# Kernel tuning notes

Hardware: AMD Instinct MI355X
Metric: run time of the kernel (lower is better)

Reference implementation:

```python
import jax, jax.numpy as jnp
import numpy as np

B, S, E = 4096, 128, 768   # batch, seq_len, bert hidden
HID = 384                  # mlp_dims[-1]
NH = 9                     # num_head (domains)
NE = 5                     # num_expert (hardcoded in module)


def setup_inputs() -> dict:
    key = jax.random.key(0)
    ks = jax.random.split(key, 14)
    std = 0.02
    return {
        "feature": jax.random.normal(ks[0], (B, S, E), dtype=jnp.float32),
        "masks": jax.random.randint(ks[1], (B, S), 0, 2, dtype=jnp.int32),
        "category": jax.random.randint(ks[2], (B,), 0, NH, dtype=jnp.int32),
        # MaskAttention: Linear(E, 1)
        "attn_w": jax.random.normal(ks[3], (E,), dtype=jnp.float32) * std,
        "attn_b": jnp.zeros((), dtype=jnp.float32),
        # gates: per-head Sequential(Linear(E,HID), ReLU, Linear(HID,NE), Softmax)
        "gate_w1": jax.random.normal(ks[4], (NH, E, HID), dtype=jnp.float32) * std,
        "gate_b1": jnp.zeros((NH, HID), dtype=jnp.float32),
        "gate_w2": jax.random.normal(ks[5], (NH, HID, NE), dtype=jnp.float32) * std,
        "gate_b2": jnp.zeros((NH, NE), dtype=jnp.float32),
        # experts: MLP(E, [HID]) = Linear(E,HID) + ReLU (dropout inactive in eval)
        "expert_w": jax.random.normal(ks[6], (NE, E, HID), dtype=jnp.float32) * std,
        "expert_b": jnp.zeros((NE, HID), dtype=jnp.float32),
        # heads: per-head Linear(HID, 1)
        "head_w": jax.random.normal(ks[7], (NH, HID), dtype=jnp.float32) * std,
        "head_b": jnp.zeros((NH,), dtype=jnp.float32),
    }


def reference(feature, masks, category, attn_w, attn_b,
              gate_w1, gate_b1, gate_w2, gate_b2,
              expert_w, expert_b, head_w, head_b):
    # ---- MaskAttention pooling: scores = Linear(E,1)(feature), mask, softmax over S
    scores = jnp.einsum('bse,e->bs', feature, attn_w) + attn_b          # [B,S]
    scores = jnp.where(masks == 0, jnp.float32(-1e9), scores)
    alpha = jax.nn.softmax(scores, axis=-1)                             # [B,S]
    pooled = jnp.einsum('bs,bse->be', alpha, feature)                   # [B,E]

    b_idx = jnp.arange(pooled.shape[0])

    # ---- category-indexed gate: compute all NH gate MLPs, select per sample
    gh = jax.nn.relu(jnp.einsum('be,heo->hbo', pooled, gate_w1) + gate_b1[:, None, :])
    glog = jnp.einsum('hbo,hok->hbk', gh, gate_w2) + gate_b2[:, None, :]
    gates_all = jax.nn.softmax(glog, axis=-1)                           # [NH,B,NE]
    gate_value = gates_all[category, b_idx]                             # [B,NE]

    # ---- experts: rep = sum_k gate[:,k] * relu(pooled @ Wk + bk)
    eh = jax.nn.relu(jnp.einsum('be,keo->kbo', pooled, expert_w) + expert_b[:, None, :])
    rep = jnp.einsum('bk,kbo->bo', gate_value, eh)                      # [B,HID]

    # ---- category-indexed head: per-sample Linear(HID,1)
    out = jnp.sum(rep * head_w[category], axis=-1) + head_b[category]   # [B]
    return jax.nn.sigmoid(out)
```

## Files before the change

kernel.cpp:

```cpp
#include <hip/hip_runtime.h>
#include <hip/hip_bf16.h>

#define Bn   4096
#define Sn   128
#define En   768
#define HIDn 384
#define NHn  9
#define NEn  5
#define MAXTILES 41

typedef __attribute__((ext_vector_type(8))) short short8;
typedef __attribute__((ext_vector_type(4))) float f32x4;

__device__ __forceinline__ unsigned short f2bf(float v) {
  unsigned int x = __float_as_uint(v);
  x += 0x7fffu + ((x >> 16) & 1u);
  return (unsigned short)(x >> 16);
}
__device__ __forceinline__ float dot4(float4 a, float4 b) {
  return fmaf(a.x, b.x, fmaf(a.y, b.y, fmaf(a.z, b.z, a.w * b.w)));
}
__device__ __forceinline__ void fma4(float4& p, float w, float4 v) {
  p.x = fmaf(w, v.x, p.x); p.y = fmaf(w, v.y, p.y);
  p.z = fmaf(w, v.z, p.z); p.w = fmaf(w, v.w, p.w);
}

__global__ __launch_bounds__(256) void prep_kernel(
    const float* __restrict__ feature, const int* __restrict__ masks,
    const float* __restrict__ attn_w, const float* __restrict__ ew,
    const float* __restrict__ g1, const int* __restrict__ category,
    unsigned short* __restrict__ pooled, unsigned short* __restrict__ Bpe,
    unsigned short* __restrict__ Bpg, int* __restrict__ rowsamp,
    int* __restrict__ meta) {
  __shared__ __align__(16) union {
    struct { float pbuf[4][768]; float sbuf[4]; } pool;
    struct { int hist[NHn][256]; int padbase[NHn]; int total[NHn];
             int tilecat[MAXTILES]; int padTiles; } srt;
  } sm;
  const int t = threadIdx.x, lane = t & 63, wid = t >> 6;
  const int bid = blockIdx.x;

  if (bid < Bn) {
    const int b = bid;
    const float4* aw = (const float4*)attn_w;
    const float4 aw0 = aw[lane], aw1 = aw[64 + lane], aw2 = aw[128 + lane];
    const float4* fb = (const float4*)(feature + (size_t)b * (Sn * En));
    unsigned long long bal = __ballot(lane < 32 && masks[b * Sn + wid * 32 + (lane & 31)] != 0);
    unsigned int m = (unsigned int)bal;
    float4 p0 = {0,0,0,0}, p1 = {0,0,0,0}, p2 = {0,0,0,0};
    float lsum = 0.f;
    if (m) {
      int s = __builtin_ctz(m); m &= m - 1;
      const float4* rp = fb + (wid * 32 + s) * (En / 4);
      float4 c0 = rp[lane], c1 = rp[64 + lane], c2 = rp[128 + lane];
      while (m) {
        int s2 = __builtin_ctz(m); m &= m - 1;
        const float4* rp2 = fb + (wid * 32 + s2) * (En / 4);
        float4 n0 = rp2[lane], n1 = rp2[64 + lane], n2 = rp2[128 + lane];
        float part = dot4(c0, aw0) + dot4(c1, aw1) + dot4(c2, aw2);
        #pragma unroll
        for (int off = 32; off; off >>= 1) part += __shfl_xor(part, off);
        float w = __expf(part);
        lsum += w;
        fma4(p0, w, c0); fma4(p1, w, c1); fma4(p2, w, c2);
        c0 = n0; c1 = n1; c2 = n2;
      }
      float part = dot4(c0, aw0) + dot4(c1, aw1) + dot4(c2, aw2);
      #pragma unroll
      for (int off = 32; off; off >>= 1) part += __shfl_xor(part, off);
      float w = __expf(part);
      lsum += w;
      fma4(p0, w, c0); fma4(p1, w, c1); fma4(p2, w, c2);
    }
    ((float4*)sm.pool.pbuf[wid])[lane] = p0;
    ((float4*)sm.pool.pbuf[wid])[64 + lane] = p1;
    ((float4*)sm.pool.pbuf[wid])[128 + lane] = p2;
    if (lane == 0) sm.pool.sbuf[wid] = lsum;
    __syncthreads();
    float total = sm.pool.sbuf[0] + sm.pool.sbuf[1] + sm.pool.sbuf[2] + sm.pool.sbuf[3];
    if (total == 0.f) {
      p0 = p1 = p2 = float4{0,0,0,0};
      for (int s = 0; s < 32; ++s) {
        const float4* rp = fb + (wid * 32 + s) * (En / 4);
        fma4(p0, 1.f, rp[lane]); fma4(p1, 1.f, rp[64 + lane]); fma4(p2, 1.f, rp[128 + lane]);
      }
      ((float4*)sm.pool.pbuf[wid])[lane] = p0;
      ((float4*)sm.pool.pbuf[wid])[64 + lane] = p1;
      ((float4*)sm.pool.pbuf[wid])[128 + lane] = p2;
      __syncthreads();
      total = 128.f;
    }
    const float inv = 1.f / total;
    if (t < 192) {
      float4 s0 = ((const float4*)sm.pool.pbuf[0])[t];
      float4 s1 = ((const float4*)sm.pool.pbuf[1])[t];
      float4 s2 = ((const float4*)sm.pool.pbuf[2])[t];
      float4 s3 = ((const float4*)sm.pool.pbuf[3])[t];
      ushort4 u;
      u.x = f2bf((s0.x+s1.x+s2.x+s3.x) * inv);
      u.y = f2bf((s0.y+s1.y+s2.y+s3.y) * inv);
      u.z = f2bf((s0.z+s1.z+s2.z+s3.z) * inv);
      u.w = f2bf((s0.w+s1.w+s2.w+s3.w) * inv);
      ((ushort4*)pooled)[(size_t)b * 192 + t] = u;
    }
    return;
  }

  if (bid < Bn + 2016) {
    const int pair = (bid - Bn) * 4 + wid;
    const int q = lane >> 4, j = lane & 15;
    const float* src; unsigned short* dst; int kt;
    if (pair < 2880) {
      int nt = pair / 24; kt = pair % 24;
      int col = nt * 16 + j;
      src = ew + (size_t)(col / HIDn) * (En * HIDn) + (col % HIDn);
      dst = Bpe + (size_t)pair * 512;
    } else {
      int g = pair - 2880;
      int h = g / 576, rem = g % 576;
      int nt = rem / 24; kt = rem % 24;
      int col = nt * 16 + j;
      src = g1 + (size_t)h * (En * HIDn) + col;
      dst = Bpg + ((size_t)(h * 24 + nt) * 24 + kt) * 512;
    }
    unsigned short outv[8] __attribute__((aligned(16)));
    #pragma unroll
    for (int e = 0; e < 8; ++e) {
      int k = kt * 32 + q * 8 + e;
      outv[e] = f2bf(src[(size_t)k * HIDn]);
    }
    *(uint4*)&dst[lane * 8] = *(const uint4*)outv;
    return;
  }

  #pragma unroll
  for (int jj = 0; jj < NHn; ++jj) sm.srt.hist[jj][t] = 0;
  __syncthreads();
  for (int i = 0; i < 16; ++i) { int c = category[t * 16 + i]; sm.srt.hist[c][t]++; }
  __syncthreads();
  if (t < NHn) {
    int run = 0;
    for (int x = 0; x < 256; ++x) { int v = sm.srt.hist[t][x]; sm.srt.hist[t][x] = run; run += v; }
    sm.srt.total[t] = run;
  }
  __syncthreads();
  if (t == 0) {
    int pb = 0, mt = 0;
    for (int jj = 0; jj < NHn; ++jj) {
      sm.srt.padbase[jj] = pb;
      int tot = sm.srt.total[jj];
      int nt = (tot + 127) >> 7;
      for (int k2 = 0; k2 < nt; ++k2) {
        meta[1 + mt + k2] = jj;
        int vv = tot - (k2 << 7); if (vv > 128) vv = 128;
        meta[64 + mt + k2] = vv;
        sm.srt.tilecat[mt + k2] = jj;
      }
      mt += nt; pb += nt << 7;
    }
    meta[0] = mt; sm.srt.padTiles = mt;
  }
  __syncthreads();
  const int padM = sm.srt.padTiles << 7;
  for (int mm = t; mm < padM; mm += 256) {
    int h = sm.srt.tilecat[mm >> 7];
    if (mm - sm.srt.padbase[h] >= sm.srt.total[h]) rowsamp[mm] = 0;
  }
  for (int i = 0; i < 16; ++i) {
    int idx = t * 16 + i; int c = category[idx];
    int off = sm.srt.hist[c][t]++;
    rowsamp[sm.srt.padbase[c] + off] = idx;
  }
}

__global__ __launch_bounds__(256) void gemm_kernel(
    const unsigned short* __restrict__ pooled, const unsigned short* __restrict__ Bpe,
    const unsigned short* __restrict__ Bpg, const float* __restrict__ eb,
    const float* __restrict__ gb1, const float* __restrict__ g2,
    const int* __restrict__ category, const float* __restrict__ hw,
    const int* __restrict__ rowsamp, const int* __restrict__ meta,
    float* __restrict__ partial, float* __restrict__ glogp) {
  __shared__ __align__(16) struct {
    unsigned short Alds[128 * 40];
    unsigned short Blds[8 * 512];
    union {
      struct { float hwlds[NHn * HIDn]; float plds[2][128]; } e;
      struct { int rs[128]; float w2lds[640]; } g;
    } u;
  } sm;
  const int t = threadIdx.x, lane = t & 63, wid = t >> 6;
  const int wm = wid >> 1, wn = wid & 1;
  const int bid = blockIdx.x;
  const int r = t >> 2, c0 = (t & 3) * 8;
  const int arow = wm * 64 + (lane & 15);
  const int aq = (lane >> 4) * 8;
  const int lrb = wm * 64 + ((lane >> 4) << 2);
  const int cb = wn * 64 + (lane & 15);
  f32x4 acc[4][4] = {};

  if (bid < 480) {
    const int bx = bid % 15, by = bid / 15;
    const int m0 = by * 128, ntg0 = bx * 8;
    for (int idx = t; idx < NHn * HIDn; idx += 256) sm.u.e.hwlds[idx] = hw[idx];
    for (int kt = 0; kt < 24; ++kt) {
      __syncthreads();
      *(uint4*)&sm.Alds[r * 40 + c0] =
          *(const uint4*)&pooled[(size_t)(m0 + r) * En + kt * 32 + c0];
      *(uint4*)&sm.Alds[(r + 64) * 40 + c0] =
          *(const uint4*)&pooled[(size_t)(m0 + r + 64) * En + kt * 32 + c0];
      #pragma unroll
      for (int rnd = 0; rnd < 2; ++rnd) {
        int chunk = t + rnd * 256;
        int nt = chunk >> 6, l2 = chunk & 63;
        *(uint4*)&sm.Blds[nt * 512 + l2 * 8] =
            *(const uint4*)&Bpe[((size_t)(ntg0 + nt) * 24 + kt) * 512 + l2 * 8];
      }
      __syncthreads();
      short8 af[4], bfv[4];
      #pragma unroll
      for (int i = 0; i < 4; ++i) af[i] = *(const short8*)&sm.Alds[(arow + i * 16) * 40 + aq];
      #pragma unroll
      for (int i = 0; i < 4; ++i) bfv[i] = *(const short8*)&sm.Blds[(wn * 4 + i) * 512 + lane * 8];
      #pragma unroll
      for (int i = 0; i < 4; ++i)
        #pragma unroll
        for (int jj = 0; jj < 4; ++jj)
          acc[i][jj] = __builtin_amdgcn_mfma_f32_16x16x32_bf16(af[i], bfv[jj], acc[i][jj], 0, 0, 0);
    }
    const int kexp = bx / 3, lcolbase = (bx % 3) * 128;
    (void)kexp;
    float sums[4][4];
    #pragma unroll
    for (int i = 0; i < 4; ++i) {
      #pragma unroll
      for (int rr = 0; rr < 4; ++rr) {
        const int row = m0 + lrb + i * 16 + rr;
        const int cat = category[row];
        float s = 0.f;
        #pragma unroll
        for (int jj = 0; jj < 4; ++jj) {
          int cl = cb + jj * 16;
          float v = acc[i][jj][rr] + eb[bx * 128 + cl];
          v = fmaxf(v, 0.f);
          s = fmaf(v, sm.u.e.hwlds[cat * HIDn + lcolbase + cl], s);
        }
        #pragma unroll
        for (int off = 8; off; off >>= 1) s += __shfl_xor(s, off);
        sums[i][rr] = s;
      }
    }
    __syncthreads();
    if ((lane & 15) == 0) {
      #pragma unroll
      for (int i = 0; i < 4; ++i)
        #pragma unroll
        for (int rr = 0; rr < 4; ++rr)
          sm.u.e.plds[wn][lrb + i * 16 + rr] = sums[i][rr];
    }
    __syncthreads();
    if (t < 128) partial[(size_t)bx * Bn + m0 + t] = sm.u.e.plds[0][t] + sm.u.e.plds[1][t];
    return;
  }

  const int gid = bid - 480;
  const int mt = gid / 3, bxg = gid % 3;
  if (mt >= meta[0]) return;
  const int h = meta[1 + mt], valid = meta[64 + mt];
  if (t < 128) sm.u.g.rs[t] = rowsamp[mt * 128 + t];
  const float* w2src = g2 + ((size_t)h * HIDn + bxg * 128) * 5;
  for (int idx = t; idx < 640; idx += 256) sm.u.g.w2lds[idx] = w2src[idx];
  for (int kt = 0; kt < 24; ++kt) {
    __syncthreads();
    *(uint4*)&sm.Alds[r * 40 + c0] =
        *(const uint4*)&pooled[(size_t)sm.u.g.rs[r] * En + kt * 32 + c0];
    *(uint4*)&sm.Alds[(r + 64) * 40 + c0] =
        *(const uint4*)&pooled[(size_t)sm.u.g.rs[r + 64] * En + kt * 32 + c0];
    #pragma unroll
    for (int rnd = 0; rnd < 2; ++rnd) {
      int chunk = t + rnd * 256;
      int nt = chunk >> 6, l2 = chunk & 63;
      *(uint4*)&sm.Blds[nt * 512 + l2 * 8] =
          *(const uint4*)&Bpg[((size_t)(h * 24 + bxg * 8 + nt) * 24 + kt) * 512 + l2 * 8];
    }
    __syncthreads();
    short8 af[4], bfv[4];
    #pragma unroll
    for (int i = 0; i < 4; ++i) af[i] = *(const short8*)&sm.Alds[(arow + i * 16) * 40 + aq];
    #pragma unroll
    for (int i = 0; i < 4; ++i) bfv[i] = *(const short8*)&sm.Blds[(wn * 4 + i) * 512 + lane * 8];
    #pragma unroll
    for (int i = 0; i < 4; ++i)
      #pragma unroll
      for (int jj = 0; jj < 4; ++jj)
        acc[i][jj] = __builtin_amdgcn_mfma_f32_16x16x32_bf16(af[i], bfv[jj], acc[i][jj], 0, 0, 0);
  }
  #pragma unroll
  for (int i = 0; i < 4; ++i) {
    #pragma unroll
    for (int rr = 0; rr < 4; ++rr) {
      const int lrow = lrb + i * 16 + rr;
      float s[5] = {0.f, 0.f, 0.f, 0.f, 0.f};
      #pragma unroll
      for (int jj = 0; jj < 4; ++jj) {
        int cl = cb + jj * 16;
        float v = acc[i][jj][rr] + gb1[h * HIDn + bxg * 128 + cl];
        v = fmaxf(v, 0.f);
        #pragma unroll
        for (int k = 0; k < 5; ++k) s[k] = fmaf(v, sm.u.g.w2lds[cl * 5 + k], s[k]);
      }
      #pragma unroll
      for (int k = 0; k < 5; ++k)
        #pragma unroll
        for (int off = 8; off; off >>= 1) s[k] += __shfl_xor(s[k], off);
      if ((lane & 15) == 0 && lrow < valid) {
        int samp = sm.u.g.rs[lrow];
        #pragma unroll
        for (int k = 0; k < 5; ++k)
          glogp[((size_t)bxg * Bn + samp) * 5 + k] = s[k];
      }
    }
  }
}

__global__ __launch_bounds__(256) void final_kernel(
    const float* __restrict__ partial, const float* __restrict__ glogp,
    const float* __restrict__ gb2, const int* __restrict__ category,
    const float* __restrict__ hb, float* __restrict__ out) {
  const int row = blockIdx.x * 256 + threadIdx.x;
  const int cat = category[row];
  float gl[5];
  #pragma unroll
  for (int k = 0; k < 5; ++k)
    gl[k] = gb2[cat * 5 + k]
          + glogp[((size_t)0 * Bn + row) * 5 + k]
          + glogp[((size_t)1 * Bn + row) * 5 + k]
          + glogp[((size_t)2 * Bn + row) * 5 + k];
  float mx = fmaxf(fmaxf(fmaxf(gl[0], gl[1]), fmaxf(gl[2], gl[3])), gl[4]);
  float ek[5], es = 0.f;
  #pragma unroll
  for (int k = 0; k < 5; ++k) { ek[k] = __expf(gl[k] - mx); es += ek[k]; }
  const float einv = 1.f / es;
  float s = 0.f;
  #pragma unroll
  for (int k = 0; k < 5; ++k) {
    float ps = partial[(size_t)(3 * k) * Bn + row]
             + partial[(size_t)(3 * k + 1) * Bn + row]
             + partial[(size_t)(3 * k + 2) * Bn + row];
    s = fmaf(ek[k] * einv, ps, s);
  }
  s += hb[cat];
  out[row] = 1.f / (1.f + __expf(-s));
}

extern "C" void kernel_launch(void* const* d_in, const int* in_sizes, int n_in,
                              void* d_out, int out_size, void* d_ws, size_t ws_size,
                              hipStream_t stream) {
  const float* feature  = (const float*)d_in[0];
  const int*   masks    = (const int*)d_in[1];
  const int*   category = (const int*)d_in[2];
  const float* attn_w   = (const float*)d_in[3];
  const float* gate_w1  = (const float*)d_in[5];
  const float* gate_b1  = (const float*)d_in[6];
  const float* gate_w2  = (const float*)d_in[7];
  const float* gate_b2  = (const float*)d_in[8];
  const float* expert_w = (const float*)d_in[9];
  const float* expert_b = (const float*)d_in[10];
  const float* head_w   = (const float*)d_in[11];
  const float* head_b   = (const float*)d_in[12];
  float* out = (float*)d_out;

  char* ws = (char*)d_ws;
  unsigned short* pooled = (unsigned short*)(ws);
  unsigned short* Bpe    = (unsigned short*)(ws + 6291456);
  unsigned short* Bpg    = (unsigned short*)(ws + 9240576);
  int* rowsamp           = (int*)(ws + 14548992);
  int* meta              = (int*)(ws + 14569984);
  float* glogp           = (float*)(ws + 14570496);
  float* partial         = (float*)(ws + 14816256);

  prep_kernel<<<dim3(Bn + 2016 + 1), dim3(256), 0, stream>>>(
      feature, masks, attn_w, expert_w, gate_w1, category,
      pooled, Bpe, Bpg, rowsamp, meta);
  gemm_kernel<<<dim3(480 + 3 * MAXTILES), dim3(256), 0, stream>>>(
      pooled, Bpe, Bpg, expert_b, gate_b1, gate_w2, category, head_w,
      rowsamp, meta, partial, glogp);
  final_kernel<<<dim3(16), dim3(256), 0, stream>>>(
      partial, glogp, gate_b2, category, head_b, out);
}
```

Baseline: 218.4 us.

## Fuse prep and GEMM into persistent kernel with atomic work queues and flags

Replaces the separate prep and GEMM launches with one persistent kernel of 768 blocks. Blocks pull work from atomic counters: first weight packing and the category sort, then attention pooling, then GEMM tiles. Each expert GEMM tile spin-waits on a per-row-tile flag, so it can start as soon as its 128 pooled rows are ready. The goal is to overlap the tail of pooling with the GEMM and remove a launch boundary, at the cost of atomic and spin-wait overhead and lower occupancy from the larger shared-memory union.

```diff
diff --git a/kernel.cpp b/kernel.cpp
--- a/kernel.cpp
+++ b/kernel.cpp
@@ -8,6 +8,14 @@
 #define NHn  9
 #define NEn  5
 #define MAXTILES 41
+#define NBLK 768
+
+#define F_PACKDONE 0
+#define F_POOLALL  1
+#define F_TILE     2
+#define F_TPREP    34
+#define F_TPOOL    35
+#define F_TGEMM    36
 
 typedef __attribute__((ext_vector_type(8))) short short8;
 typedef __attribute__((ext_vector_type(4))) float f32x4;
@@ -24,24 +32,120 @@
   p.x = fmaf(w, v.x, p.x); p.y = fmaf(w, v.y, p.y);
   p.z = fmaf(w, v.z, p.z); p.w = fmaf(w, v.w, p.w);
 }
-
-__global__ __launch_bounds__(256) void prep_kernel(
+__device__ __forceinline__ int aload(int* p) {
+  return __hip_atomic_load(p, __ATOMIC_ACQUIRE, __HIP_MEMORY_SCOPE_AGENT);
+}
+__device__ __forceinline__ int aadd(int* p, int v) {
+  return __hip_atomic_fetch_add(p, v, __ATOMIC_RELEASE, __HIP_MEMORY_SCOPE_AGENT);
+}
+
+union SM {
+  struct { float pbuf[4][768]; float sbuf[4]; } pool;
+  struct { int hist[NHn][256]; int padbase[NHn]; int total[NHn];
+           int tilecat[MAXTILES]; int padTiles; } srt;
+  struct { unsigned short Alds[128 * 40]; unsigned short Blds[8 * 512];
+           union { struct { float hwlds[NHn * HIDn]; float plds[2][128]; } e;
+                   struct { int rs[128]; float w2lds[640]; } g; } u; } gemm;
+};
+
+__global__ void zero_kernel(int* __restrict__ flags) { flags[threadIdx.x] = 0; }
+
+__global__ __launch_bounds__(256, 2) void mega_kernel(
     const float* __restrict__ feature, const int* __restrict__ masks,
     const float* __restrict__ attn_w, const float* __restrict__ ew,
     const float* __restrict__ g1, const int* __restrict__ category,
+    const float* __restrict__ gb1, const float* __restrict__ g2,
+    const float* __restrict__ eb, const float* __restrict__ hw,
     unsigned short* __restrict__ pooled, unsigned short* __restrict__ Bpe,
     unsigned short* __restrict__ Bpg, int* __restrict__ rowsamp,
-    int* __restrict__ meta) {
-  __shared__ __align__(16) union {
-    struct { float pbuf[4][768]; float sbuf[4]; } pool;
-    struct { int hist[NHn][256]; int padbase[NHn]; int total[NHn];
-             int tilecat[MAXTILES]; int padTiles; } srt;
-  } sm;
+    int* __restrict__ meta, float* __restrict__ partial,
+    float* __restrict__ glogp, int* __restrict__ flags) {
+  __shared__ SM sm;
+  __shared__ int curu;
   const int t = threadIdx.x, lane = t & 63, wid = t >> 6;
-  const int bid = blockIdx.x;
-
-  if (bid < Bn) {
-    const int b = bid;
+
+  int nmine = 0;
+  for (;;) {
+    __syncthreads();
+    if (t == 0) curu = __hip_atomic_fetch_add(&flags[F_TPREP], 1, __ATOMIC_RELAXED, __HIP_MEMORY_SCOPE_AGENT);
+    __syncthreads();
+    const int u = curu;
+    if (u >= 2017) break;
+    ++nmine;
+    if (u < 2016) {
+      const int pair = u * 4 + wid;
+      const int q = lane >> 4, j = lane & 15;
+      const float* src; unsigned short* dst; int kt;
+      if (pair < 2880) {
+        int nt = pair / 24; kt = pair % 24;
+        int col = nt * 16 + j;
+        src = ew + (size_t)(col / HIDn) * (En * HIDn) + (col % HIDn);
+        dst = Bpe + (size_t)pair * 512;
+      } else {
+        int g = pair - 2880;
+        int h = g / 576, rem = g % 576;
+        int nt = rem / 24; kt = rem % 24;
+        int col = nt * 16 + j;
+        src = g1 + (size_t)h * (En * HIDn) + col;
+        dst = Bpg + ((size_t)(h * 24 + nt) * 24 + kt) * 512;
+      }
+      unsigned short outv[8] __attribute__((aligned(16)));
+      #pragma unroll
+      for (int e = 0; e < 8; ++e) {
+        int k = kt * 32 + q * 8 + e;
+        outv[e] = f2bf(src[(size_t)k * HIDn]);
+      }
+      *(uint4*)&dst[lane * 8] = *(const uint4*)outv;
+    } else {
+      #pragma unroll
+      for (int jj = 0; jj < NHn; ++jj) sm.srt.hist[jj][t] = 0;
+      __syncthreads();
+      for (int i = 0; i < 16; ++i) { int c = category[t * 16 + i]; sm.srt.hist[c][t]++; }
+      __syncthreads();
+      if (t < NHn) {
+        int run = 0;
+        for (int x = 0; x < 256; ++x) { int v = sm.srt.hist[t][x]; sm.srt.hist[t][x] = run; run += v; }
+        sm.srt.total[t] = run;
+      }
+      __syncthreads();
+      if (t == 0) {
+        int pb = 0, mt = 0;
+        for (int jj = 0; jj < NHn; ++jj) {
+          sm.srt.padbase[jj] = pb;
+          int tot = sm.srt.total[jj];
+          int nt = (tot + 127) >> 7;
+          for (int k2 = 0; k2 < nt; ++k2) {
+            meta[1 + mt + k2] = jj;
+            int vv = tot - (k2 << 7); if (vv > 128) vv = 128;
+            meta[64 + mt + k2] = vv;
+            sm.srt.tilecat[mt + k2] = jj;
+          }
+          mt += nt; pb += nt << 7;
+        }
+        meta[0] = mt; sm.srt.padTiles = mt;
+      }
+      __syncthreads();
+      const int padM = sm.srt.padTiles << 7;
+      for (int mm = t; mm < padM; mm += 256) {
+        int h = sm.srt.tilecat[mm >> 7];
+        if (mm - sm.srt.padbase[h] >= sm.srt.total[h]) rowsamp[mm] = 0;
+      }
+      for (int i = 0; i < 16; ++i) {
+        int idx = t * 16 + i; int c = category[idx];
+        int off = sm.srt.hist[c][t]++;
+        rowsamp[sm.srt.padbase[c] + off] = idx;
+      }
+    }
+  }
+  __syncthreads();
+  if (t == 0) { __threadfence(); aadd(&flags[F_PACKDONE], nmine); }
+
+  for (;;) {
+    __syncthreads();
+    if (t == 0) curu = __hip_atomic_fetch_add(&flags[F_TPOOL], 1, __ATOMIC_RELAXED, __HIP_MEMORY_SCOPE_AGENT);
+    __syncthreads();
+    const int b = curu;
+    if (b >= Bn) break;
     const float4* aw = (const float4*)attn_w;
     const float4 aw0 = aw[lane], aw1 = aw[64 + lane], aw2 = aw[128 + lane];
     const float4* fb = (const float4*)(feature + (size_t)b * (Sn * En));
@@ -96,227 +200,165 @@
       float4 s1 = ((const float4*)sm.pool.pbuf[1])[t];
       float4 s2 = ((const float4*)sm.pool.pbuf[2])[t];
       float4 s3 = ((const float4*)sm.pool.pbuf[3])[t];
-      ushort4 u;
-      u.x = f2bf((s0.x+s1.x+s2.x+s3.x) * inv);
-      u.y = f2bf((s0.y+s1.y+s2.y+s3.y) * inv);
-      u.z = f2bf((s0.z+s1.z+s2.z+s3.z) * inv);
-      u.w = f2bf((s0.w+s1.w+s2.w+s3.w) * inv);
-      ((ushort4*)pooled)[(size_t)b * 192 + t] = u;
-    }
-    return;
+      ushort4 u4;
+      u4.x = f2bf((s0.x+s1.x+s2.x+s3.x) * inv);
+      u4.y = f2bf((s0.y+s1.y+s2.y+s3.y) * inv);
+      u4.z = f2bf((s0.z+s1.z+s2.z+s3.z) * inv);
+      u4.w = f2bf((s0.w+s1.w+s2.w+s3.w) * inv);
+      ((ushort4*)pooled)[(size_t)b * 192 + t] = u4;
+    }
+    __syncthreads();
+    if (t == 0) {
+      __threadfence();
+      aadd(&flags[F_TILE + (b >> 7)], 1);
+      aadd(&flags[F_POOLALL], 1);
+    }
   }
 
-  if (bid < Bn + 2016) {
-    const int pair = (bid - Bn) * 4 + wid;
-    const int q = lane >> 4, j = lane & 15;
-    const float* src; unsigned short* dst; int kt;
-    if (pair < 2880) {
-      int nt = pair / 24; kt = pair % 24;
-      int col = nt * 16 + j;
-      src = ew + (size_t)(col / HIDn) * (En * HIDn) + (col % HIDn);
-      dst = Bpe + (size_t)pair * 512;
-    } else {
-      int g = pair - 2880;
-      int h = g / 576, rem = g % 576;
-      int nt = rem / 24; kt = rem % 24;
-      int col = nt * 16 + j;
-      src = g1 + (size_t)h * (En * HIDn) + col;
-      dst = Bpg + ((size_t)(h * 24 + nt) * 24 + kt) * 512;
-    }
-    unsigned short outv[8] __attribute__((aligned(16)));
-    #pragma unroll
-    for (int e = 0; e < 8; ++e) {
-      int k = kt * 32 + q * 8 + e;
-      outv[e] = f2bf(src[(size_t)k * HIDn]);
-    }
-    *(uint4*)&dst[lane * 8] = *(const uint4*)outv;
-    return;
-  }
-
-  #pragma unroll
-  for (int jj = 0; jj < NHn; ++jj) sm.srt.hist[jj][t] = 0;
-  __syncthreads();
-  for (int i = 0; i < 16; ++i) { int c = category[t * 16 + i]; sm.srt.hist[c][t]++; }
-  __syncthreads();
-  if (t < NHn) {
-    int run = 0;
-    for (int x = 0; x < 256; ++x) { int v = sm.srt.hist[t][x]; sm.srt.hist[t][x] = run; run += v; }
-    sm.srt.total[t] = run;
-  }
-  __syncthreads();
-  if (t == 0) {
-    int pb = 0, mt = 0;
-    for (int jj = 0; jj < NHn; ++jj) {
-      sm.srt.padbase[jj] = pb;
-      int tot = sm.srt.total[jj];
-      int nt = (tot + 127) >> 7;
-      for (int k2 = 0; k2 < nt; ++k2) {
-        meta[1 + mt + k2] = jj;
-        int vv = tot - (k2 << 7); if (vv > 128) vv = 128;
-        meta[64 + mt + k2] = vv;
-        sm.srt.tilecat[mt + k2] = jj;
-      }
-      mt += nt; pb += nt << 7;
-    }
-    meta[0] = mt; sm.srt.padTiles = mt;
-  }
-  __syncthreads();
-  const int padM = sm.srt.padTiles << 7;
-  for (int mm = t; mm < padM; mm += 256) {
-    int h = sm.srt.tilecat[mm >> 7];
-    if (mm - sm.srt.padbase[h] >= sm.srt.total[h]) rowsamp[mm] = 0;
-  }
-  for (int i = 0; i < 16; ++i) {
-    int idx = t * 16 + i; int c = category[idx];
-    int off = sm.srt.hist[c][t]++;
-    rowsamp[sm.srt.padbase[c] + off] = idx;
-  }
-}
-
-__global__ __launch_bounds__(256) void gemm_kernel(
-    const unsigned short* __restrict__ pooled, const unsigned short* __restrict__ Bpe,
-    const unsigned short* __restrict__ Bpg, const float* __restrict__ eb,
-    const float* __restrict__ gb1, const float* __restrict__ g2,
-    const int* __restrict__ category, const float* __restrict__ hw,
-    const int* __restrict__ rowsamp, const int* __restrict__ meta,
-    float* __restrict__ partial, float* __restrict__ glogp) {
-  __shared__ __align__(16) struct {
-    unsigned short Alds[128 * 40];
-    unsigned short Blds[8 * 512];
-    union {
-      struct { float hwlds[NHn * HIDn]; float plds[2][128]; } e;
-      struct { int rs[128]; float w2lds[640]; } g;
-    } u;
-  } sm;
-  const int t = threadIdx.x, lane = t & 63, wid = t >> 6;
+  const int r = t >> 2, c0i = (t & 3) * 8;
   const int wm = wid >> 1, wn = wid & 1;
-  const int bid = blockIdx.x;
-  const int r = t >> 2, c0 = (t & 3) * 8;
   const int arow = wm * 64 + (lane & 15);
   const int aq = (lane >> 4) * 8;
   const int lrb = wm * 64 + ((lane >> 4) << 2);
   const int cb = wn * 64 + (lane & 15);
-  f32x4 acc[4][4] = {};
-
-  if (bid < 480) {
-    const int bx = bid % 15, by = bid / 15;
-    const int m0 = by * 128, ntg0 = bx * 8;
-    for (int idx = t; idx < NHn * HIDn; idx += 256) sm.u.e.hwlds[idx] = hw[idx];
-    for (int kt = 0; kt < 24; ++kt) {
-      __syncthreads();
-      *(uint4*)&sm.Alds[r * 40 + c0] =
-          *(const uint4*)&pooled[(size_t)(m0 + r) * En + kt * 32 + c0];
-      *(uint4*)&sm.Alds[(r + 64) * 40 + c0] =
-          *(const uint4*)&pooled[(size_t)(m0 + r + 64) * En + kt * 32 + c0];
+  for (;;) {
+    __syncthreads();
+    if (t == 0) curu = __hip_atomic_fetch_add(&flags[F_TGEMM], 1, __ATOMIC_RELAXED, __HIP_MEMORY_SCOPE_AGENT);
+    __syncthreads();
+    const int u = curu;
+    if (u >= 480 + 3 * MAXTILES) break;
+    f32x4 acc[4][4] = {};
+    if (u < 480) {
+      const int bx = u % 15, by = u / 15;
+      if (t == 0) {
+        while (aload(&flags[F_PACKDONE]) < 2017 || aload(&flags[F_TILE + by]) < 128)
+          __builtin_amdgcn_s_sleep(8);
+        __threadfence();
+      }
+      __syncthreads();
+      const int m0 = by * 128, ntg0 = bx * 8;
+      for (int idx = t; idx < NHn * HIDn; idx += 256) sm.gemm.u.e.hwlds[idx] = hw[idx];
+      for (int kt = 0; kt < 24; ++kt) {
+        __syncthreads();
+        *(uint4*)&sm.gemm.Alds[r * 40 + c0i] =
+            *(const uint4*)&pooled[(size_t)(m0 + r) * En + kt * 32 + c0i];
+        *(uint4*)&sm.gemm.Alds[(r + 64) * 40 + c0i] =
+            *(const uint4*)&pooled[(size_t)(m0 + r + 64) * En + kt * 32 + c0i];
+        #pragma unroll
+        for (int rnd = 0; rnd < 2; ++rnd) {
+          int chunk = t + rnd * 256;
+          int nt = chunk >> 6, l2 = chunk & 63;
+          *(uint4*)&sm.gemm.Blds[nt * 512 + l2 * 8] =
+              *(const uint4*)&Bpe[((size_t)(ntg0 + nt) * 24 + kt) * 512 + l2 * 8];
+        }
+        __syncthreads();
+        short8 af[4], bfv[4];
+        #pragma unroll
+        for (int i = 0; i < 4; ++i) af[i] = *(const short8*)&sm.gemm.Alds[(arow + i * 16) * 40 + aq];
+        #pragma unroll
+        for (int i = 0; i < 4; ++i) bfv[i] = *(const short8*)&sm.gemm.Blds[(wn * 4 + i) * 512 + lane * 8];
+        #pragma unroll
+        for (int i = 0; i < 4; ++i)
+          #pragma unroll
+          for (int jj = 0; jj < 4; ++jj)
+            acc[i][jj] = __builtin_amdgcn_mfma_f32_16x16x32_bf16(af[i], bfv[jj], acc[i][jj], 0, 0, 0);
+      }
+      const int lcolbase = (bx % 3) * 128;
+      float sums[4][4];
       #pragma unroll
-      for (int rnd = 0; rnd < 2; ++rnd) {
-        int chunk = t + rnd * 256;
-        int nt = chunk >> 6, l2 = chunk & 63;
-        *(uint4*)&sm.Blds[nt * 512 + l2 * 8] =
-            *(const uint4*)&Bpe[((size_t)(ntg0 + nt) * 24 + kt) * 512 + l2 * 8];
-      }
-      __syncthreads();
-      short8 af[4], bfv[4];
-      #pragma unroll
-      for (int i = 0; i < 4; ++i) af[i] = *(const short8*)&sm.Alds[(arow + i * 16) * 40 + aq];
-      #pragma unroll
-      for (int i = 0; i < 4; ++i) bfv[i] = *(const short8*)&sm.Blds[(wn * 4 + i) * 512 + lane * 8];
-      #pragma unroll
-      for (int i = 0; i < 4; ++i)
-        #pragma unroll
-        for (int jj = 0; jj < 4; ++jj)
-          acc[i][jj] = __builtin_amdgcn_mfma_f32_16x16x32_bf16(af[i], bfv[jj], acc[i][jj], 0, 0, 0);
-    }
-    const int kexp = bx / 3, lcolbase = (bx % 3) * 128;
-    (void)kexp;
-    float sums[4][4];
-    #pragma unroll
-    for (int i = 0; i < 4; ++i) {
-      #pragma unroll
-      for (int rr = 0; rr < 4; ++rr) {
-        const int row = m0 + lrb + i * 16 + rr;
-        const int cat = category[row];
-        float s = 0.f;
-        #pragma unroll
-        for (int jj = 0; jj < 4; ++jj) {
-          int cl = cb + jj * 16;
-          float v = acc[i][jj][rr] + eb[bx * 128 + cl];
-          v = fmaxf(v, 0.f);
-          s = fmaf(v, sm.u.e.hwlds[cat * HIDn + lcolbase + cl], s);
+      for (int i = 0; i < 4; ++i) {
+        #pragma unroll
+        for (int rr = 0; rr < 4; ++rr) {
+          const int row = m0 + lrb + i * 16 + rr;
+          const int cat = category[row];
+          float s = 0.f;
+          #pragma unroll
+          for (int jj = 0; jj < 4; ++jj) {
+            int cl = cb + jj * 16;
+            float v = acc[i][jj][rr] + eb[bx * 128 + cl];
+            v = fmaxf(v, 0.f);
+            s = fmaf(v, sm.gemm.u.e.hwlds[cat * HIDn + lcolbase + cl], s);
+          }
+          #pragma unroll
+          for (int off = 8; off; off >>= 1) s += __shfl_xor(s, off);
+          sums[i][rr] = s;
         }
-        #pragma unroll
-        for (int off = 8; off; off >>= 1) s += __shfl_xor(s, off);
-        sums[i][rr] = s;
-      }
-    }
-    __syncthreads();
-    if ((lane & 15) == 0) {
-      #pragma unroll
-      for (int i = 0; i < 4; ++i)
-        #pragma unroll
-        for (int rr = 0; rr < 4; ++rr)
-          sm.u.e.plds[wn][lrb + i * 16 + rr] = sums[i][rr];
-    }
-    __syncthreads();
-    if (t < 128) partial[(size_t)bx * Bn + m0 + t] = sm.u.e.plds[0][t] + sm.u.e.plds[1][t];
-    return;
-  }
-
-  const int gid = bid - 480;
-  const int mt = gid / 3, bxg = gid % 3;
-  if (mt >= meta[0]) return;
-  const int h = meta[1 + mt], valid = meta[64 + mt];
-  if (t < 128) sm.u.g.rs[t] = rowsamp[mt * 128 + t];
-  const float* w2src = g2 + ((size_t)h * HIDn + bxg * 128) * 5;
-  for (int idx = t; idx < 640; idx += 256) sm.u.g.w2lds[idx] = w2src[idx];
-  for (int kt = 0; kt < 24; ++kt) {
-    __syncthreads();
-    *(uint4*)&sm.Alds[r * 40 + c0] =
-        *(const uint4*)&pooled[(size_t)sm.u.g.rs[r] * En + kt * 32 + c0];
-    *(uint4*)&sm.Alds[(r + 64) * 40 + c0] =
-        *(const uint4*)&pooled[(size_t)sm.u.g.rs[r + 64] * En + kt * 32 + c0];
-    #pragma unroll
-    for (int rnd = 0; rnd < 2; ++rnd) {
-      int chunk = t + rnd * 256;
-      int nt = chunk >> 6, l2 = chunk & 63;
-      *(uint4*)&sm.Blds[nt * 512 + l2 * 8] =
-          *(const uint4*)&Bpg[((size_t)(h * 24 + bxg * 8 + nt) * 24 + kt) * 512 + l2 * 8];
-    }
-    __syncthreads();
-    short8 af[4], bfv[4];
-    #pragma unroll
-    for (int i = 0; i < 4; ++i) af[i] = *(const short8*)&sm.Alds[(arow + i * 16) * 40 + aq];
-    #pragma unroll
-    for (int i = 0; i < 4; ++i) bfv[i] = *(const short8*)&sm.Blds[(wn * 4 + i) * 512 + lane * 8];
-    #pragma unroll
-    for (int i = 0; i < 4; ++i)
-      #pragma unroll
-      for (int jj = 0; jj < 4; ++jj)
-        acc[i][jj] = __builtin_amdgcn_mfma_f32_16x16x32_bf16(af[i], bfv[jj], acc[i][jj], 0, 0, 0);
-  }
-  #pragma unroll
-  for (int i = 0; i < 4; ++i) {
-    #pragma unroll
-    for (int rr = 0; rr < 4; ++rr) {
-      const int lrow = lrb + i * 16 + rr;
-      float s[5] = {0.f, 0.f, 0.f, 0.f, 0.f};
-      #pragma unroll
-      for (int jj = 0; jj < 4; ++jj) {
-        int cl = cb + jj * 16;
-        float v = acc[i][jj][rr] + gb1[h * HIDn + bxg * 128 + cl];
-        v = fmaxf(v, 0.f);
-        #pragma unroll
-        for (int k = 0; k < 5; ++k) s[k] = fmaf(v, sm.u.g.w2lds[cl * 5 + k], s[k]);
-      }
-      #pragma unroll
-      for (int k = 0; k < 5; ++k)
-        #pragma unroll
-        for (int off = 8; off; off >>= 1) s[k] += __shfl_xor(s[k], off);
-      if ((lane & 15) == 0 && lrow < valid) {
-        int samp = sm.u.g.rs[lrow];
-        #pragma unroll
-        for (int k = 0; k < 5; ++k)
-          glogp[((size_t)bxg * Bn + samp) * 5 + k] = s[k];
+      }
+      __syncthreads();
+      if ((lane & 15) == 0) {
+        #pragma unroll
+        for (int i = 0; i < 4; ++i)
+          #pragma unroll
+          for (int rr = 0; rr < 4; ++rr)
+            sm.gemm.u.e.plds[wn][lrb + i * 16 + rr] = sums[i][rr];
+      }
+      __syncthreads();
+      if (t < 128) partial[(size_t)bx * Bn + m0 + t] = sm.gemm.u.e.plds[0][t] + sm.gemm.u.e.plds[1][t];
+    } else {
+      const int gid = u - 480;
+      const int mt = gid / 3, bxg = gid % 3;
+      if (t == 0) {
+        while (aload(&flags[F_PACKDONE]) < 2017 || aload(&flags[F_POOLALL]) < Bn)
+          __builtin_amdgcn_s_sleep(8);
+        __threadfence();
+      }
+      __syncthreads();
+      if (mt < meta[0]) {
+        const int h = meta[1 + mt], valid = meta[64 + mt];
+        if (t < 128) sm.gemm.u.g.rs[t] = rowsamp[mt * 128 + t];
+        const float* w2src = g2 + ((size_t)h * HIDn + bxg * 128) * 5;
+        for (int idx = t; idx < 640; idx += 256) sm.gemm.u.g.w2lds[idx] = w2src[idx];
+        for (int kt = 0; kt < 24; ++kt) {
+          __syncthreads();
+          *(uint4*)&sm.gemm.Alds[r * 40 + c0i] =
+              *(const uint4*)&pooled[(size_t)sm.gemm.u.g.rs[r] * En + kt * 32 + c0i];
+          *(uint4*)&sm.gemm.Alds[(r + 64) * 40 + c0i] =
+              *(const uint4*)&pooled[(size_t)sm.gemm.u.g.rs[r + 64] * En + kt * 32 + c0i];
+          #pragma unroll
+          for (int rnd = 0; rnd < 2; ++rnd) {
+            int chunk = t + rnd * 256;
+            int nt = chunk >> 6, l2 = chunk & 63;
+            *(uint4*)&sm.gemm.Blds[nt * 512 + l2 * 8] =
+                *(const uint4*)&Bpg[((size_t)(h * 24 + bxg * 8 + nt) * 24 + kt) * 512 + l2 * 8];
+          }
+          __syncthreads();
+          short8 af[4], bfv[4];
+          #pragma unroll
+          for (int i = 0; i < 4; ++i) af[i] = *(const short8*)&sm.gemm.Alds[(arow + i * 16) * 40 + aq];
+          #pragma unroll
+          for (int i = 0; i < 4; ++i) bfv[i] = *(const short8*)&sm.gemm.Blds[(wn * 4 + i) * 512 + lane * 8];
+          #pragma unroll
+          for (int i = 0; i < 4; ++i)
+            #pragma unroll
+            for (int jj = 0; jj < 4; ++jj)
+              acc[i][jj] = __builtin_amdgcn_mfma_f32_16x16x32_bf16(af[i], bfv[jj], acc[i][jj], 0, 0, 0);
+        }
+        #pragma unroll
+        for (int i = 0; i < 4; ++i) {
+          #pragma unroll
+          for (int rr = 0; rr < 4; ++rr) {
+            const int lrow = lrb + i * 16 + rr;
+            float s[5] = {0.f, 0.f, 0.f, 0.f, 0.f};
+            #pragma unroll
+            for (int jj = 0; jj < 4; ++jj) {
+              int cl = cb + jj * 16;
+              float v = acc[i][jj][rr] + gb1[h * HIDn + bxg * 128 + cl];
+              v = fmaxf(v, 0.f);
+              #pragma unroll
+              for (int k = 0; k < 5; ++k) s[k] = fmaf(v, sm.gemm.u.g.w2lds[cl * 5 + k], s[k]);
+            }
+            #pragma unroll
+            for (int k = 0; k < 5; ++k)
+              #pragma unroll
+              for (int off = 8; off; off >>= 1) s[k] += __shfl_xor(s[k], off);
+            if ((lane & 15) == 0 && lrow < valid) {
+              int samp = sm.gemm.u.g.rs[lrow];
+              #pragma unroll
+              for (int k = 0; k < 5; ++k)
+                glogp[((size_t)bxg * Bn + samp) * 5 + k] = s[k];
+            }
+          }
+        }
       }
     }
   }
@@ -377,13 +419,13 @@
   int* meta              = (int*)(ws + 14569984);
   float* glogp           = (float*)(ws + 14570496);
   float* partial         = (float*)(ws + 14816256);
-
-  prep_kernel<<<dim3(Bn + 2016 + 1), dim3(256), 0, stream>>>(
+  int* flags             = (int*)(ws + 15062016);
+
+  zero_kernel<<<dim3(1), dim3(64), 0, stream>>>(flags);
+  mega_kernel<<<dim3(NBLK), dim3(256), 0, stream>>>(
       feature, masks, attn_w, expert_w, gate_w1, category,
-      pooled, Bpe, Bpg, rowsamp, meta);
-  gemm_kernel<<<dim3(480 + 3 * MAXTILES), dim3(256), 0, stream>>>(
-      pooled, Bpe, Bpg, expert_b, gate_b1, gate_w2, category, head_w,
-      rowsamp, meta, partial, glogp);
+      gate_b1, gate_w2, expert_b, head_w,
+      pooled, Bpe, Bpg, rowsamp, meta, partial, glogp, flags);
   final_kernel<<<dim3(16), dim3(256), 0, stream>>>(
       partial, glogp, gate_b2, category, head_b, out);
 }
```

Result: slower. 820.7 us (+275.8%).

## Pre-pack pooled activations into MFMA fragment layout and load tiles via global_load_lds

Applied to the files above, without the earlier changes.

The prep kernel now also writes the pooled bf16 activations in the same 16x32 fragment-packed layout used for the expert weights. The expert GEMM then loads both A and B tiles directly into LDS with the global_load_lds builtin, when available, instead of routing them through registers with padded row-major copies. The head-weight LDS staging is dropped in favour of direct global reads in the epilogue. This adds an extra 6 MB write in prep and enlarges the workspace, in exchange for a cheaper, register-free tile load loop.

```diff
diff --git a/kernel.cpp b/kernel.cpp
--- a/kernel.cpp
+++ b/kernel.cpp
@@ -25,13 +25,24 @@
   p.z = fmaf(w, v.z, p.z); p.w = fmaf(w, v.w, p.w);
 }
 
+#if defined(__has_builtin) && __has_builtin(__builtin_amdgcn_global_load_lds)
+#define HAVE_GLOAD_LDS 1
+__device__ __forceinline__ void gload16(const unsigned short* g, unsigned short* l) {
+  __builtin_amdgcn_global_load_lds(
+      (const __attribute__((address_space(1))) unsigned int*)g,
+      (__attribute__((address_space(3))) unsigned int*)l, 16, 0, 0);
+}
+#else
+#define HAVE_GLOAD_LDS 0
+#endif
+
 __global__ __launch_bounds__(256) void prep_kernel(
     const float* __restrict__ feature, const int* __restrict__ masks,
     const float* __restrict__ attn_w, const float* __restrict__ ew,
     const float* __restrict__ g1, const int* __restrict__ category,
-    unsigned short* __restrict__ pooled, unsigned short* __restrict__ Bpe,
-    unsigned short* __restrict__ Bpg, int* __restrict__ rowsamp,
-    int* __restrict__ meta) {
+    unsigned short* __restrict__ pooled, unsigned short* __restrict__ Ape,
+    unsigned short* __restrict__ Bpe, unsigned short* __restrict__ Bpg,
+    int* __restrict__ rowsamp, int* __restrict__ meta) {
   __shared__ __align__(16) union {
     struct { float pbuf[4][768]; float sbuf[4]; } pool;
     struct { int hist[NHn][256]; int padbase[NHn]; int total[NHn];
@@ -96,12 +107,14 @@
       float4 s1 = ((const float4*)sm.pool.pbuf[1])[t];
       float4 s2 = ((const float4*)sm.pool.pbuf[2])[t];
       float4 s3 = ((const float4*)sm.pool.pbuf[3])[t];
-      ushort4 u;
-      u.x = f2bf((s0.x+s1.x+s2.x+s3.x) * inv);
-      u.y = f2bf((s0.y+s1.y+s2.y+s3.y) * inv);
-      u.z = f2bf((s0.z+s1.z+s2.z+s3.z) * inv);
-      u.w = f2bf((s0.w+s1.w+s2.w+s3.w) * inv);
-      ((ushort4*)pooled)[(size_t)b * 192 + t] = u;
+      ushort4 u4;
+      u4.x = f2bf((s0.x+s1.x+s2.x+s3.x) * inv);
+      u4.y = f2bf((s0.y+s1.y+s2.y+s3.y) * inv);
+      u4.z = f2bf((s0.z+s1.z+s2.z+s3.z) * inv);
+      u4.w = f2bf((s0.w+s1.w+s2.w+s3.w) * inv);
+      ((ushort4*)pooled)[(size_t)b * 192 + t] = u4;
+      const int kt = t >> 3, q = (t >> 1) & 3, e = (t & 1) * 4;
+      *(ushort4*)&Ape[((size_t)(b >> 4) * 24 + kt) * 512 + ((b & 15) + (q << 4)) * 8 + e] = u4;
     }
     return;
   }
@@ -174,26 +187,21 @@
 }
 
 __global__ __launch_bounds__(256) void gemm_kernel(
-    const unsigned short* __restrict__ pooled, const unsigned short* __restrict__ Bpe,
-    const unsigned short* __restrict__ Bpg, const float* __restrict__ eb,
-    const float* __restrict__ gb1, const float* __restrict__ g2,
-    const int* __restrict__ category, const float* __restrict__ hw,
-    const int* __restrict__ rowsamp, const int* __restrict__ meta,
-    float* __restrict__ partial, float* __restrict__ glogp) {
-  __shared__ __align__(16) struct {
-    unsigned short Alds[128 * 40];
-    unsigned short Blds[8 * 512];
-    union {
-      struct { float hwlds[NHn * HIDn]; float plds[2][128]; } e;
-      struct { int rs[128]; float w2lds[640]; } g;
-    } u;
+    const unsigned short* __restrict__ pooled, const unsigned short* __restrict__ Ape,
+    const unsigned short* __restrict__ Bpe, const unsigned short* __restrict__ Bpg,
+    const float* __restrict__ eb, const float* __restrict__ gb1,
+    const float* __restrict__ g2, const int* __restrict__ category,
+    const float* __restrict__ hw, const int* __restrict__ rowsamp,
+    const int* __restrict__ meta, float* __restrict__ partial,
+    float* __restrict__ glogp) {
+  __shared__ __align__(16) union {
+    struct { unsigned short Af[4096]; unsigned short Bf[4096]; float plds[2][128]; } e;
+    struct { unsigned short Ap[128 * 40]; unsigned short Bf[4096];
+             int rs[128]; float w2[640]; } g;
   } sm;
   const int t = threadIdx.x, lane = t & 63, wid = t >> 6;
   const int wm = wid >> 1, wn = wid & 1;
   const int bid = blockIdx.x;
-  const int r = t >> 2, c0 = (t & 3) * 8;
-  const int arow = wm * 64 + (lane & 15);
-  const int aq = (lane >> 4) * 8;
   const int lrb = wm * 64 + ((lane >> 4) << 2);
   const int cb = wn * 64 + (lane & 15);
   f32x4 acc[4][4] = {};
@@ -201,34 +209,34 @@
   if (bid < 480) {
     const int bx = bid % 15, by = bid / 15;
     const int m0 = by * 128, ntg0 = bx * 8;
-    for (int idx = t; idx < NHn * HIDn; idx += 256) sm.u.e.hwlds[idx] = hw[idx];
     for (int kt = 0; kt < 24; ++kt) {
       __syncthreads();
-      *(uint4*)&sm.Alds[r * 40 + c0] =
-          *(const uint4*)&pooled[(size_t)(m0 + r) * En + kt * 32 + c0];
-      *(uint4*)&sm.Alds[(r + 64) * 40 + c0] =
-          *(const uint4*)&pooled[(size_t)(m0 + r + 64) * En + kt * 32 + c0];
       #pragma unroll
       for (int rnd = 0; rnd < 2; ++rnd) {
-        int chunk = t + rnd * 256;
-        int nt = chunk >> 6, l2 = chunk & 63;
-        *(uint4*)&sm.Blds[nt * 512 + l2 * 8] =
-            *(const uint4*)&Bpe[((size_t)(ntg0 + nt) * 24 + kt) * 512 + l2 * 8];
+        const int st = wid * 2 + rnd;
+#if HAVE_GLOAD_LDS
+        gload16(&Ape[((size_t)(by * 8 + st) * 24 + kt) * 512 + lane * 8], &sm.e.Af[st * 512]);
+        gload16(&Bpe[((size_t)(ntg0 + st) * 24 + kt) * 512 + lane * 8], &sm.e.Bf[st * 512]);
+#else
+        *(uint4*)&sm.e.Af[st * 512 + lane * 8] =
+            *(const uint4*)&Ape[((size_t)(by * 8 + st) * 24 + kt) * 512 + lane * 8];
+        *(uint4*)&sm.e.Bf[st * 512 + lane * 8] =
+            *(const uint4*)&Bpe[((size_t)(ntg0 + st) * 24 + kt) * 512 + lane * 8];
+#endif
       }
       __syncthreads();
       short8 af[4], bfv[4];
       #pragma unroll
-      for (int i = 0; i < 4; ++i) af[i] = *(const short8*)&sm.Alds[(arow + i * 16) * 40 + aq];
-      #pragma unroll
-      for (int i = 0; i < 4; ++i) bfv[i] = *(const short8*)&sm.Blds[(wn * 4 + i) * 512 + lane * 8];
+      for (int i = 0; i < 4; ++i) af[i] = *(const short8*)&sm.e.Af[(wm * 4 + i) * 512 + lane * 8];
+      #pragma unroll
+      for (int i = 0; i < 4; ++i) bfv[i] = *(const short8*)&sm.e.Bf[(wn * 4 + i) * 512 + lane * 8];
       #pragma unroll
       for (int i = 0; i < 4; ++i)
         #pragma unroll
         for (int jj = 0; jj < 4; ++jj)
           acc[i][jj] = __builtin_amdgcn_mfma_f32_16x16x32_bf16(af[i], bfv[jj], acc[i][jj], 0, 0, 0);
     }
-    const int kexp = bx / 3, lcolbase = (bx % 3) * 128;
-    (void)kexp;
+    const int lcolbase = (bx % 3) * 128;
     float sums[4][4];
     #pragma unroll
     for (int i = 0; i < 4; ++i) {
@@ -242,7 +250,7 @@
           int cl = cb + jj * 16;
           float v = acc[i][jj][rr] + eb[bx * 128 + cl];
           v = fmaxf(v, 0.f);
-          s = fmaf(v, sm.u.e.hwlds[cat * HIDn + lcolbase + cl], s);
+          s = fmaf(v, hw[cat * HIDn + lcolbase + cl], s);
         }
         #pragma unroll
         for (int off = 8; off; off >>= 1) s += __shfl_xor(s, off);
@@ -255,10 +263,10 @@
       for (int i = 0; i < 4; ++i)
         #pragma unroll
         for (int rr = 0; rr < 4; ++rr)
-          sm.u.e.plds[wn][lrb + i * 16 + rr] = sums[i][rr];
+          sm.e.plds[wn][lrb + i * 16 + rr] = sums[i][rr];
     }
     __syncthreads();
-    if (t < 128) partial[(size_t)bx * Bn + m0 + t] = sm.u.e.plds[0][t] + sm.u.e.plds[1][t];
+    if (t < 128) partial[(size_t)bx * Bn + m0 + t] = sm.e.plds[0][t] + sm.e.plds[1][t];
     return;
   }
 
@@ -266,28 +274,34 @@
   const int mt = gid / 3, bxg = gid % 3;
   if (mt >= meta[0]) return;
   const int h = meta[1 + mt], valid = meta[64 + mt];
-  if (t < 128) sm.u.g.rs[t] = rowsamp[mt * 128 + t];
+  const int r = t >> 2, c0i = (t & 3) * 8;
+  const int arow = wm * 64 + (lane & 15);
+  const int aq = (lane >> 4) * 8;
+  if (t < 128) sm.g.rs[t] = rowsamp[mt * 128 + t];
   const float* w2src = g2 + ((size_t)h * HIDn + bxg * 128) * 5;
-  for (int idx = t; idx < 640; idx += 256) sm.u.g.w2lds[idx] = w2src[idx];
+  for (int idx = t; idx < 640; idx += 256) sm.g.w2[idx] = w2src[idx];
   for (int kt = 0; kt < 24; ++kt) {
     __syncthreads();
-    *(uint4*)&sm.Alds[r * 40 + c0] =
-        *(const uint4*)&pooled[(size_t)sm.u.g.rs[r] * En + kt * 32 + c0];
-    *(uint4*)&sm.Alds[(r + 64) * 40 + c0] =
-        *(const uint4*)&pooled[(size_t)sm.u.g.rs[r + 64] * En + kt * 32 + c0];
+    *(uint4*)&sm.g.Ap[r * 40 + c0i] =
+        *(const uint4*)&pooled[(size_t)sm.g.rs[r] * En + kt * 32 + c0i];
+    *(uint4*)&sm.g.Ap[(r + 64) * 40 + c0i] =
+        *(const uint4*)&pooled[(size_t)sm.g.rs[r + 64] * En + kt * 32 + c0i];
     #pragma unroll
     for (int rnd = 0; rnd < 2; ++rnd) {
-      int chunk = t + rnd * 256;
-      int nt = chunk >> 6, l2 = chunk & 63;
-      *(uint4*)&sm.Blds[nt * 512 + l2 * 8] =
-          *(const uint4*)&Bpg[((size_t)(h * 24 + bxg * 8 + nt) * 24 + kt) * 512 + l2 * 8];
+      const int st = wid * 2 + rnd;
+#if HAVE_GLOAD_LDS
+      gload16(&Bpg[((size_t)(h * 24 + bxg * 8 + st) * 24 + kt) * 512 + lane * 8], &sm.g.Bf[st * 512]);
+#else
+      *(uint4*)&sm.g.Bf[st * 512 + lane * 8] =
+          *(const uint4*)&Bpg[((size_t)(h * 24 + bxg * 8 + st) * 24 + kt) * 512 + lane * 8];
+#endif
     }
     __syncthreads();
     short8 af[4], bfv[4];
     #pragma unroll
-    for (int i = 0; i < 4; ++i) af[i] = *(const short8*)&sm.Alds[(arow + i * 16) * 40 + aq];
-    #pragma unroll
-    for (int i = 0; i < 4; ++i) bfv[i] = *(const short8*)&sm.Blds[(wn * 4 + i) * 512 + lane * 8];
+    for (int i = 0; i < 4; ++i) af[i] = *(const short8*)&sm.g.Ap[(arow + i * 16) * 40 + aq];
+    #pragma unroll
+    for (int i = 0; i < 4; ++i) bfv[i] = *(const short8*)&sm.g.Bf[(wn * 4 + i) * 512 + lane * 8];
     #pragma unroll
     for (int i = 0; i < 4; ++i)
       #pragma unroll
@@ -306,14 +320,14 @@
         float v = acc[i][jj][rr] + gb1[h * HIDn + bxg * 128 + cl];
         v = fmaxf(v, 0.f);
         #pragma unroll
-        for (int k = 0; k < 5; ++k) s[k] = fmaf(v, sm.u.g.w2lds[cl * 5 + k], s[k]);
+        for (int k = 0; k < 5; ++k) s[k] = fmaf(v, sm.g.w2[cl * 5 + k], s[k]);
       }
       #pragma unroll
       for (int k = 0; k < 5; ++k)
         #pragma unroll
         for (int off = 8; off; off >>= 1) s[k] += __shfl_xor(s[k], off);
       if ((lane & 15) == 0 && lrow < valid) {
-        int samp = sm.u.g.rs[lrow];
+        int samp = sm.g.rs[lrow];
         #pragma unroll
         for (int k = 0; k < 5; ++k)
           glogp[((size_t)bxg * Bn + samp) * 5 + k] = s[k];
@@ -371,18 +385,19 @@
 
   char* ws = (char*)d_ws;
   unsigned short* pooled = (unsigned short*)(ws);
-  unsigned short* Bpe    = (unsigned short*)(ws + 6291456);
-  unsigned short* Bpg    = (unsigned short*)(ws + 9240576);
-  int* rowsamp           = (int*)(ws + 14548992);
-  int* meta              = (int*)(ws + 14569984);
-  float* glogp           = (float*)(ws + 14570496);
-  float* partial         = (float*)(ws + 14816256);
+  unsigned short* Ape    = (unsigned short*)(ws + 6291456);
+  unsigned short* Bpe    = (unsigned short*)(ws + 12582912);
+  unsigned short* Bpg    = (unsigned short*)(ws + 15532032);
+  int* rowsamp           = (int*)(ws + 20840448);
+  int* meta              = (int*)(ws + 20861440);
+  float* glogp           = (float*)(ws + 20861952);
+  float* partial         = (float*)(ws + 21107712);
 
   prep_kernel<<<dim3(Bn + 2016 + 1), dim3(256), 0, stream>>>(
       feature, masks, attn_w, expert_w, gate_w1, category,
-      pooled, Bpe, Bpg, rowsamp, meta);
+      pooled, Ape, Bpe, Bpg, rowsamp, meta);
   gemm_kernel<<<dim3(480 + 3 * MAXTILES), dim3(256), 0, stream>>>(
-      pooled, Bpe, Bpg, expert_b, gate_b1, gate_w2, category, head_w,
+      pooled, Ape, Bpe, Bpg, expert_b, gate_b1, gate_w2, category, head_w,
       rowsamp, meta, partial, glogp);
   final_kernel<<<dim3(16), dim3(256), 0, stream>>>(
       partial, glogp, gate_b2, category, head_b, out);
```

After: 230.9 us. 1.06x slower.
